# Optimization experiments

Measured on AMD Instinct MI355X. Metric: run time of the kernel, lower is better.

Reference implementation:

```python
import jax, jax.numpy as jnp
import numpy as np

N = 10000
E = 320000
IN, HID, OUT = 512, 128, 128
HEADS, GC = 4, 64
NEG_SLOPE = 0.2


def setup_inputs() -> dict:
    key = jax.random.key(0)
    ks = jax.random.split(key, 12)
    inp = {
        'x': jax.random.normal(ks[0], (N, IN), dtype=jnp.float32),
        'edge_index': jax.random.randint(ks[1], (2, E), 0, N, dtype=jnp.int64),
        # encoder params
        'W1': jax.random.normal(ks[2], (IN, HID), dtype=jnp.float32) / np.sqrt(IN),
        'b1': jnp.zeros((HID,), dtype=jnp.float32),
        'W2': jax.random.normal(ks[3], (HID, OUT), dtype=jnp.float32) / np.sqrt(HID),
        'b2': jnp.zeros((OUT,), dtype=jnp.float32),
        # GATConv params: lin weight [OUT, HEADS*GC], att vectors [HEADS, GC], bias [HEADS*GC]
        'Wg': jax.random.normal(ks[4], (OUT, HEADS * GC), dtype=jnp.float32) / np.sqrt(OUT),
        'att_src': jax.random.normal(ks[5], (HEADS, GC), dtype=jnp.float32) * 0.1,
        'att_dst': jax.random.normal(ks[6], (HEADS, GC), dtype=jnp.float32) * 0.1,
        'bias_g': jnp.zeros((HEADS * GC,), dtype=jnp.float32),
    }
    return inp


def _forward(x, W1, b1, W2, b2, Wg, att_src, att_dst, bias_g, edge_index):
    # encoder: Linear -> ReLU -> Linear
    h = jax.nn.relu(x @ W1 + b1) @ W2 + b2  # [N, OUT]
    # GATConv adds self-loops by default
    loops = jnp.arange(N, dtype=edge_index.dtype)
    src = jnp.concatenate([edge_index[0], loops])  # message sources j
    dst = jnp.concatenate([edge_index[1], loops])  # message targets i
    # per-head linear transform
    g = (h @ Wg).reshape(N, HEADS, GC)  # [N, H, C]
    a_src = jnp.sum(g * att_src, axis=-1)  # [N, H]
    a_dst = jnp.sum(g * att_dst, axis=-1)  # [N, H]
    e = a_src[src] + a_dst[dst]            # [E+N, H]
    e = jax.nn.leaky_relu(e, NEG_SLOPE)
    # segment softmax over incoming edges of each destination node
    m = jax.ops.segment_max(e, dst, num_segments=N)  # [N, H]
    ex = jnp.exp(e - m[dst])
    s = jax.ops.segment_sum(ex, dst, num_segments=N)  # [N, H]
    alpha = ex / s[dst]                    # [E+N, H]
    # weighted scatter-aggregate of source features
    out = jax.ops.segment_sum(g[src] * alpha[:, :, None], dst, num_segments=N)  # [N, H, C]
    return out.reshape(N, HEADS * GC) + bias_g


def reference(x, edge_index, W1, b1, W2, b2, Wg, att_src, att_dst, bias_g):
    return _forward(x, W1, b1, W2, b2, Wg, att_src, att_dst, bias_g, edge_index)
```

## Files before the change

kernel.cpp:

```cpp
#include <hip/hip_runtime.h>

#define N_NODES 10000
#define N_EDGES 320000
#define DIM_IN  512
#define DIM_HID 128
#define HC      256
#define NEG_SLOPE 0.2f
#define SLOT    96

typedef short short8 __attribute__((ext_vector_type(8)));
typedef float floatx4 __attribute__((ext_vector_type(4)));

__device__ __forceinline__ unsigned short f2bf(float x) {
  unsigned int u = __float_as_uint(x);
  u += 0x7FFFu + ((u >> 16) & 1u);
  return (unsigned short)(u >> 16);
}

union Sm1 {
  struct { unsigned short As[64][48]; unsigned short Bs[32][48]; } g;
  struct { float Ast[16][68]; float Bsf[16][64]; } p;
};

__global__ __launch_bounds__(256) void fused1_kernel(
    const float* __restrict__ x, const float* __restrict__ W1,
    const float* __restrict__ b1,
    const float* __restrict__ W2, const float* __restrict__ Wg,
    const float* __restrict__ b2,
    unsigned short* __restrict__ h1b, unsigned short* __restrict__ WfT,
    float* __restrict__ bfuse, int* __restrict__ cursor) {
  __shared__ Sm1 sm;
  const int t = threadIdx.x;
  const int b = blockIdx.x;

  if (b < 628) {
    constexpr int K = DIM_IN, N = DIM_HID, BK = 32;
    const int m0 = (b % 157) * 64, n0 = (b / 157) * 32;
    const int w = t >> 6, L = t & 63, lm = L & 15, q = L >> 4;
    floatx4 acc[2] = {};
    const int ar = t >> 3, ac = (t & 7) * 4;
    float4 va0, va1, vb, va0n, va1n, vbn;
    auto ld = [&](int kb, float4& a0, float4& a1, float4& bw) {
      a0 = (m0 + ar < N_NODES)
          ? *(const float4*)(x + (size_t)(m0 + ar) * K + kb + ac)
          : make_float4(0.f, 0.f, 0.f, 0.f);
      a1 = (m0 + ar + 32 < N_NODES)
          ? *(const float4*)(x + (size_t)(m0 + ar + 32) * K + kb + ac)
          : make_float4(0.f, 0.f, 0.f, 0.f);
      bw = *(const float4*)(W1 + (size_t)(kb + ar) * N + n0 + ac);
    };
    constexpr int NT = K / BK;
    ld(0, va0, va1, vb);
    for (int kt = 0; kt < NT; ++kt) {
      ushort4 s0 = {f2bf(va0.x), f2bf(va0.y), f2bf(va0.z), f2bf(va0.w)};
      ushort4 s1 = {f2bf(va1.x), f2bf(va1.y), f2bf(va1.z), f2bf(va1.w)};
      *(ushort4*)&sm.g.As[ar][ac]      = s0;
      *(ushort4*)&sm.g.As[ar + 32][ac] = s1;
      sm.g.Bs[ac + 0][ar] = f2bf(vb.x);
      sm.g.Bs[ac + 1][ar] = f2bf(vb.y);
      sm.g.Bs[ac + 2][ar] = f2bf(vb.z);
      sm.g.Bs[ac + 3][ar] = f2bf(vb.w);
      __syncthreads();
      if (kt + 1 < NT) ld((kt + 1) * BK, va0n, va1n, vbn);
      const short8 af = *(const short8*)&sm.g.As[w * 16 + lm][q * 8];
#pragma unroll
      for (int nt = 0; nt < 2; ++nt) {
        const short8 bf = *(const short8*)&sm.g.Bs[nt * 16 + lm][q * 8];
        acc[nt] = __builtin_amdgcn_mfma_f32_16x16x32_bf16(af, bf, acc[nt], 0, 0, 0);
      }
      __syncthreads();
      va0 = va0n; va1 = va1n; vb = vbn;
    }
    const int row0 = m0 + w * 16 + q * 4;
#pragma unroll
    for (int nt = 0; nt < 2; ++nt) {
      const int col = n0 + nt * 16 + lm;
      const float bv = b1[col];
#pragma unroll
      for (int r = 0; r < 4; ++r)
        if (row0 + r < N_NODES)
          h1b[(size_t)(row0 + r) * N + col] = f2bf(fmaxf(acc[nt][r] + bv, 0.f));
    }
    return;
  }

  const int bp = b - 628;
  {
    const int flat = bp * 256 + t;
    if (flat < (N_NODES + 3) / 4) ((int4*)cursor)[flat] = make_int4(0, 0, 0, 0);
  }
  const int bx = bp >> 2, by = bp & 3;
  const int tx = t & 15, ty = t >> 4;
  const int m0 = bx * 64, n0 = by * 64;
  const int ar = t >> 2, ac4 = (t & 3) * 4;
  const int br = t >> 4, bc4 = (t & 15) * 4;
  const int arow = m0 + ar;
  float acc[4][4] = {};
  float4 av, bv, avn, bvn;
  auto gload = [&](int k0, float4& a4, float4& b4) {
    if (arow < DIM_HID)       a4 = *(const float4*)(W2 + (size_t)arow * DIM_HID + k0 + ac4);
    else if (arow == DIM_HID) a4 = *(const float4*)(b2 + k0 + ac4);
    else                      a4 = make_float4(0.f, 0.f, 0.f, 0.f);
    b4 = *(const float4*)(Wg + (size_t)(k0 + br) * HC + n0 + bc4);
  };
  gload(0, av, bv);
  for (int k0 = 0; k0 < DIM_HID; k0 += 16) {
    sm.p.Ast[ac4 + 0][ar] = av.x; sm.p.Ast[ac4 + 1][ar] = av.y;
    sm.p.Ast[ac4 + 2][ar] = av.z; sm.p.Ast[ac4 + 3][ar] = av.w;
    *(float4*)&sm.p.Bsf[br][bc4] = bv;
    __syncthreads();
    if (k0 + 16 < DIM_HID) gload(k0 + 16, avn, bvn);
#pragma unroll
    for (int kk = 0; kk < 16; ++kk) {
      const float4 a = *(const float4*)&sm.p.Ast[kk][ty * 4];
      const float4 bq = *(const float4*)&sm.p.Bsf[kk][tx * 4];
      const float as[4] = {a.x, a.y, a.z, a.w};
      const float bs[4] = {bq.x, bq.y, bq.z, bq.w};
#pragma unroll
      for (int i = 0; i < 4; ++i)
#pragma unroll
        for (int j = 0; j < 4; ++j) acc[i][j] = fmaf(as[i], bs[j], acc[i][j]);
    }
    __syncthreads();
    av = avn; bv = bvn;
  }
#pragma unroll
  for (int i = 0; i < 4; ++i) {
    const int row = m0 + ty * 4 + i;
#pragma unroll
    for (int j = 0; j < 4; ++j) {
      const int col = n0 + tx * 4 + j;
      if (row < DIM_HID)       WfT[(size_t)col * DIM_HID + row] = f2bf(acc[i][j]);
      else if (row == DIM_HID) bfuse[col] = acc[i][j];
    }
  }
}

__global__ __launch_bounds__(256) void gemm2_kernel(
    const unsigned short* __restrict__ h1b, const unsigned short* __restrict__ WfT,
    const float* __restrict__ bfuse, unsigned short* __restrict__ g,
    const float* __restrict__ att_src, const float* __restrict__ att_dst,
    float* __restrict__ a_src, float* __restrict__ a_dst,
    const int* __restrict__ e_src, const int* __restrict__ e_dst,
    int* __restrict__ cursor, int* __restrict__ src_sorted) {
  constexpr int K = DIM_HID, N = HC, BK = 32;
  __shared__ unsigned short As[64][48];
  __shared__ unsigned short Bs[64][48];
  const int t = threadIdx.x;
  {
    const int nthr = gridDim.x * gridDim.y * 256;
    const int flat = (blockIdx.y * gridDim.x + blockIdx.x) * 256 + t;
    for (int id = flat; id < N_EDGES + N_NODES; id += nthr) {
      int s, d;
      if (id < N_EDGES) { s = e_src[id]; d = e_dst[id]; }
      else              { s = d = id - N_EDGES; }
      src_sorted[d * SLOT + atomicAdd(&cursor[d], 1)] = s;
    }
  }
  const int m0 = blockIdx.x * 64, n0 = blockIdx.y * 64;
  const int w = t >> 6, L = t & 63, lm = L & 15, q = L >> 4;
  floatx4 acc[4] = {};
  uint4 ab, abn, bb, bbn;
  auto ld = [&](int kb, uint4& va, uint4& vb) {
    va = *(const uint4*)(h1b + (size_t)(m0 + (t >> 2)) * K + kb + (t & 3) * 8);
    vb = *(const uint4*)(WfT + (size_t)(n0 + (t >> 2)) * K + kb + (t & 3) * 8);
  };
  constexpr int NT = K / BK;
  ld(0, ab, bb);
  for (int kt = 0; kt < NT; ++kt) {
    *(uint4*)&As[t >> 2][(t & 3) * 8] = ab;
    *(uint4*)&Bs[t >> 2][(t & 3) * 8] = bb;
    __syncthreads();
    if (kt + 1 < NT) ld((kt + 1) * BK, abn, bbn);
    const short8 af = *(const short8*)&As[w * 16 + lm][q * 8];
#pragma unroll
    for (int nt = 0; nt < 4; ++nt) {
      const short8 bf = *(const short8*)&Bs[nt * 16 + lm][q * 8];
      acc[nt] = __builtin_amdgcn_mfma_f32_16x16x32_bf16(af, bf, acc[nt], 0, 0, 0);
    }
    __syncthreads();
    ab = abn; bb = bbn;
  }
  const int row0 = m0 + w * 16 + q * 4;
  const int hh = n0 >> 6;
  float ps[4] = {}, pd[4] = {};
#pragma unroll
  for (int nt = 0; nt < 4; ++nt) {
    const int col = n0 + nt * 16 + lm;
    const float bv = bfuse[col];
    const float as_c = att_src[hh * 64 + nt * 16 + lm];
    const float ad_c = att_dst[hh * 64 + nt * 16 + lm];
#pragma unroll
    for (int r = 0; r < 4; ++r) {
      const float gv = acc[nt][r] + bv;
      if (row0 + r < N_NODES) g[(size_t)(row0 + r) * N + col] = f2bf(gv);
      ps[r] = fmaf(gv, as_c, ps[r]);
      pd[r] = fmaf(gv, ad_c, pd[r]);
    }
  }
#pragma unroll
  for (int r = 0; r < 4; ++r) {
#pragma unroll
    for (int off = 1; off < 16; off <<= 1) {
      ps[r] += __shfl_xor(ps[r], off);
      pd[r] += __shfl_xor(pd[r], off);
    }
    if (lm == 0 && row0 + r < N_NODES) {
      a_src[(row0 + r) * 4 + hh] = ps[r];
      a_dst[(row0 + r) * 4 + hh] = pd[r];
    }
  }
}

__global__ __launch_bounds__(256) void aggregate_kernel(
    const unsigned short* __restrict__ g, const float* __restrict__ a_src,
    const float* __restrict__ a_dst, const int* __restrict__ cursor,
    const int* __restrict__ src_sorted, const float* __restrict__ bias_g,
    float* __restrict__ out) {
  const int wv   = threadIdx.x >> 6;
  const int lane = threadIdx.x & 63;
  const int node = blockIdx.x * 4 + wv;
  if (node >= N_NODES) return;
  const int e2 = lane >> 5;
  const int c8 = lane & 31;
  const int h  = c8 >> 3;
  const int start = node * SLOT;
  const int end   = start + cursor[node];
  const float4 ad = *(const float4*)(a_dst + node * 4);

  float a[8] = {};
  float s_loc = 0.f;
  for (int base = start; base < end; base += 64) {
    const int rem = min(64, end - base);
    int   sidxL = 0;
    float w0 = 0.f, w1 = 0.f, w2 = 0.f, w3 = 0.f;
    if (lane < rem) {
      sidxL = src_sorted[base + lane];
      const float4 as4 = *(const float4*)(a_src + sidxL * 4);
      float e0 = as4.x + ad.x; e0 = (e0 > 0.f) ? e0 : NEG_SLOPE * e0;
      float e1 = as4.y + ad.y; e1 = (e1 > 0.f) ? e1 : NEG_SLOPE * e1;
      float ee = as4.z + ad.z; ee = (ee > 0.f) ? ee : NEG_SLOPE * ee;
      float e3 = as4.w + ad.w; e3 = (e3 > 0.f) ? e3 : NEG_SLOPE * e3;
      w0 = __expf(e0); w1 = __expf(e1); w2 = __expf(ee); w3 = __expf(e3);
    }
    const int half = (rem + 1) >> 1;
#pragma unroll 4
    for (int k = 0; k < half; ++k) {
      const int j  = 2 * k + e2;
      const int js = (j < rem) ? j : (rem - 1);
      const int sj = __shfl(sidxL, js);
      const float f0 = __shfl(w0, js), f1 = __shfl(w1, js);
      const float f2 = __shfl(w2, js), f3 = __shfl(w3, js);
      float w = (h & 2) ? ((h & 1) ? f3 : f2) : ((h & 1) ? f1 : f0);
      if (j >= rem) w = 0.f;
      const uint4 gv = *(const uint4*)(g + (size_t)sj * HC + c8 * 8);
      s_loc += w;
      a[0] = fmaf(w, __uint_as_float(gv.x << 16), a[0]);
      a[1] = fmaf(w, __uint_as_float(gv.x & 0xFFFF0000u), a[1]);
      a[2] = fmaf(w, __uint_as_float(gv.y << 16), a[2]);
      a[3] = fmaf(w, __uint_as_float(gv.y & 0xFFFF0000u), a[3]);
      a[4] = fmaf(w, __uint_as_float(gv.z << 16), a[4]);
      a[5] = fmaf(w, __uint_as_float(gv.z & 0xFFFF0000u), a[5]);
      a[6] = fmaf(w, __uint_as_float(gv.w << 16), a[6]);
      a[7] = fmaf(w, __uint_as_float(gv.w & 0xFFFF0000u), a[7]);
    }
  }
#pragma unroll
  for (int k = 0; k < 8; ++k) a[k] += __shfl_xor(a[k], 32);
  s_loc += __shfl_xor(s_loc, 32);
  if (e2 == 0) {
    const float inv = 1.f / s_loc;
    const float4 b0 = *(const float4*)(bias_g + c8 * 8);
    const float4 b1v = *(const float4*)(bias_g + c8 * 8 + 4);
    float4 o0, o1;
    o0.x = a[0] * inv + b0.x;  o0.y = a[1] * inv + b0.y;
    o0.z = a[2] * inv + b0.z;  o0.w = a[3] * inv + b0.w;
    o1.x = a[4] * inv + b1v.x; o1.y = a[5] * inv + b1v.y;
    o1.z = a[6] * inv + b1v.z; o1.w = a[7] * inv + b1v.w;
    float* op = out + (size_t)node * HC + c8 * 8;
    *(float4*)op = o0;
    *(float4*)(op + 4) = o1;
  }
}

extern "C" void kernel_launch(void* const* d_in, const int* in_sizes, int n_in,
                              void* d_out, int out_size, void* d_ws, size_t ws_size,
                              hipStream_t stream) {
  const float* x       = (const float*)d_in[0];
  const int*   ei      = (const int*)d_in[1];
  const float* W1      = (const float*)d_in[2];
  const float* b1      = (const float*)d_in[3];
  const float* W2      = (const float*)d_in[4];
  const float* b2      = (const float*)d_in[5];
  const float* Wg      = (const float*)d_in[6];
  const float* att_src = (const float*)d_in[7];
  const float* att_dst = (const float*)d_in[8];
  const float* bias_g  = (const float*)d_in[9];
  float* out = (float*)d_out;

  char* ws = (char*)d_ws;
  unsigned short* h1b = (unsigned short*)ws; ws += (size_t)(N_NODES + 64) * DIM_HID * 2;
  unsigned short* g   = (unsigned short*)ws; ws += (size_t)N_NODES * HC * 2;
  unsigned short* WfT = (unsigned short*)ws; ws += (size_t)HC * DIM_HID * 2;
  float* bfuse   = (float*)ws; ws += (size_t)HC * 4;
  float* a_src   = (float*)ws; ws += (size_t)N_NODES * 4 * 4;
  float* a_dst   = (float*)ws; ws += (size_t)N_NODES * 4 * 4;
  int* cursor    = (int*)ws;   ws += (size_t)N_NODES * 4;
  int* src_sorted= (int*)ws;   ws += (size_t)N_NODES * SLOT * 4;

  const dim3 blk(256);
  fused1_kernel<<<640, blk, 0, stream>>>(
      x, W1, b1, W2, Wg, b2, h1b, WfT, bfuse, cursor);
  gemm2_kernel<<<dim3(157, 4), blk, 0, stream>>>(
      h1b, WfT, bfuse, g, att_src, att_dst, a_src, a_dst,
      ei, ei + N_EDGES, cursor, src_sorted);
  aggregate_kernel<<<(N_NODES + 3) / 4, blk, 0, stream>>>(
      g, a_src, a_dst, cursor, src_sorted, bias_g, out);
}
```

Before: 152.7 us.

## Stage edge weights in LDS and gather four edges per wave step

The aggregation kernel now computes each edge's softmax numerators and source index once per wave, stores them in shared memory, and reads them back. This replaces the per-edge shuffle broadcasts. Each lane now covers 16 channels with two 16-byte loads, so one wave processes four edges per iteration instead of two, which adds gather parallelism. The cost is more registers for the wider accumulator, an extra cross-lane reduction step, and a block-wide barrier. The node bounds check is removed, which depends on N being a multiple of 4 and on degree never exceeding SLOT.

New measurement: 147.5 us. -3.4%, faster.

```diff
diff --git a/kernel.cpp b/kernel.cpp
--- a/kernel.cpp
+++ b/kernel.cpp
@@ -217,69 +217,87 @@
     const float* __restrict__ a_dst, const int* __restrict__ cursor,
     const int* __restrict__ src_sorted, const float* __restrict__ bias_g,
     float* __restrict__ out) {
+  __shared__ int   s_idx[4][SLOT];
+  __shared__ float s_w[4][SLOT * 4];
   const int wv   = threadIdx.x >> 6;
   const int lane = threadIdx.x & 63;
   const int node = blockIdx.x * 4 + wv;
-  if (node >= N_NODES) return;
-  const int e2 = lane >> 5;
-  const int c8 = lane & 31;
-  const int h  = c8 >> 3;
   const int start = node * SLOT;
-  const int end   = start + cursor[node];
+  const int deg   = cursor[node];
+  const int degp  = (deg + 3) & ~3;
   const float4 ad = *(const float4*)(a_dst + node * 4);
 
-  float a[8] = {};
-  float s_loc = 0.f;
-  for (int base = start; base < end; base += 64) {
-    const int rem = min(64, end - base);
-    int   sidxL = 0;
+  for (int j = lane; j < degp; j += 64) {
+    int   s  = 0;
     float w0 = 0.f, w1 = 0.f, w2 = 0.f, w3 = 0.f;
-    if (lane < rem) {
-      sidxL = src_sorted[base + lane];
-      const float4 as4 = *(const float4*)(a_src + sidxL * 4);
+    if (j < deg) {
+      s = src_sorted[start + j];
+      const float4 as4 = *(const float4*)(a_src + s * 4);
       float e0 = as4.x + ad.x; e0 = (e0 > 0.f) ? e0 : NEG_SLOPE * e0;
       float e1 = as4.y + ad.y; e1 = (e1 > 0.f) ? e1 : NEG_SLOPE * e1;
-      float ee = as4.z + ad.z; ee = (ee > 0.f) ? ee : NEG_SLOPE * ee;
+      float e2v = as4.z + ad.z; e2v = (e2v > 0.f) ? e2v : NEG_SLOPE * e2v;
       float e3 = as4.w + ad.w; e3 = (e3 > 0.f) ? e3 : NEG_SLOPE * e3;
-      w0 = __expf(e0); w1 = __expf(e1); w2 = __expf(ee); w3 = __expf(e3);
-    }
-    const int half = (rem + 1) >> 1;
-#pragma unroll 4
-    for (int k = 0; k < half; ++k) {
-      const int j  = 2 * k + e2;
-      const int js = (j < rem) ? j : (rem - 1);
-      const int sj = __shfl(sidxL, js);
-      const float f0 = __shfl(w0, js), f1 = __shfl(w1, js);
-      const float f2 = __shfl(w2, js), f3 = __shfl(w3, js);
-      float w = (h & 2) ? ((h & 1) ? f3 : f2) : ((h & 1) ? f1 : f0);
-      if (j >= rem) w = 0.f;
-      const uint4 gv = *(const uint4*)(g + (size_t)sj * HC + c8 * 8);
-      s_loc += w;
-      a[0] = fmaf(w, __uint_as_float(gv.x << 16), a[0]);
-      a[1] = fmaf(w, __uint_as_float(gv.x & 0xFFFF0000u), a[1]);
-      a[2] = fmaf(w, __uint_as_float(gv.y << 16), a[2]);
-      a[3] = fmaf(w, __uint_as_float(gv.y & 0xFFFF0000u), a[3]);
-      a[4] = fmaf(w, __uint_as_float(gv.z << 16), a[4]);
-      a[5] = fmaf(w, __uint_as_float(gv.z & 0xFFFF0000u), a[5]);
-      a[6] = fmaf(w, __uint_as_float(gv.w << 16), a[6]);
-      a[7] = fmaf(w, __uint_as_float(gv.w & 0xFFFF0000u), a[7]);
-    }
-  }
-#pragma unroll
-  for (int k = 0; k < 8; ++k) a[k] += __shfl_xor(a[k], 32);
+      w0 = __expf(e0); w1 = __expf(e1); w2 = __expf(e2v); w3 = __expf(e3);
+    }
+    s_idx[wv][j] = s;
+    float* wp = &s_w[wv][j * 4];
+    wp[0] = w0; wp[1] = w1; wp[2] = w2; wp[3] = w3;
+  }
+  __syncthreads();
+
+  const int e4 = lane >> 4;
+  const int c4 = lane & 15;
+  const int h  = c4 >> 2;
+  const unsigned short* gbase = g + (size_t)c4 * 16;
+  float a[16] = {};
+  float s_loc = 0.f;
+  const int iters = degp >> 2;
+#pragma unroll 2
+  for (int k = 0; k < iters; ++k) {
+    const int j  = 4 * k + e4;
+    const int sj = s_idx[wv][j];
+    const float w = s_w[wv][j * 4 + h];
+    const uint4 g0 = *(const uint4*)(gbase + (size_t)sj * HC);
+    const uint4 g1 = *(const uint4*)(gbase + (size_t)sj * HC + 8);
+    s_loc += w;
+    a[0]  = fmaf(w, __uint_as_float(g0.x << 16),         a[0]);
+    a[1]  = fmaf(w, __uint_as_float(g0.x & 0xFFFF0000u), a[1]);
+    a[2]  = fmaf(w, __uint_as_float(g0.y << 16),         a[2]);
+    a[3]  = fmaf(w, __uint_as_float(g0.y & 0xFFFF0000u), a[3]);
+    a[4]  = fmaf(w, __uint_as_float(g0.z << 16),         a[4]);
+    a[5]  = fmaf(w, __uint_as_float(g0.z & 0xFFFF0000u), a[5]);
+    a[6]  = fmaf(w, __uint_as_float(g0.w << 16),         a[6]);
+    a[7]  = fmaf(w, __uint_as_float(g0.w & 0xFFFF0000u), a[7]);
+    a[8]  = fmaf(w, __uint_as_float(g1.x << 16),         a[8]);
+    a[9]  = fmaf(w, __uint_as_float(g1.x & 0xFFFF0000u), a[9]);
+    a[10] = fmaf(w, __uint_as_float(g1.y << 16),         a[10]);
+    a[11] = fmaf(w, __uint_as_float(g1.y & 0xFFFF0000u), a[11]);
+    a[12] = fmaf(w, __uint_as_float(g1.z << 16),         a[12]);
+    a[13] = fmaf(w, __uint_as_float(g1.z & 0xFFFF0000u), a[13]);
+    a[14] = fmaf(w, __uint_as_float(g1.w << 16),         a[14]);
+    a[15] = fmaf(w, __uint_as_float(g1.w & 0xFFFF0000u), a[15]);
+  }
+#pragma unroll
+  for (int k = 0; k < 16; ++k) {
+    a[k] += __shfl_xor(a[k], 16);
+    a[k] += __shfl_xor(a[k], 32);
+  }
+  s_loc += __shfl_xor(s_loc, 16);
   s_loc += __shfl_xor(s_loc, 32);
-  if (e2 == 0) {
+  if (e4 == 0) {
     const float inv = 1.f / s_loc;
-    const float4 b0 = *(const float4*)(bias_g + c8 * 8);
-    const float4 b1v = *(const float4*)(bias_g + c8 * 8 + 4);
-    float4 o0, o1;
-    o0.x = a[0] * inv + b0.x;  o0.y = a[1] * inv + b0.y;
-    o0.z = a[2] * inv + b0.z;  o0.w = a[3] * inv + b0.w;
-    o1.x = a[4] * inv + b1v.x; o1.y = a[5] * inv + b1v.y;
-    o1.z = a[6] * inv + b1v.z; o1.w = a[7] * inv + b1v.w;
-    float* op = out + (size_t)node * HC + c8 * 8;
-    *(float4*)op = o0;
-    *(float4*)(op + 4) = o1;
+    float* op = out + (size_t)node * HC + c4 * 16;
+    const float* bp = bias_g + c4 * 16;
+#pragma unroll
+    for (int q = 0; q < 4; ++q) {
+      const float4 bq = *(const float4*)(bp + q * 4);
+      float4 o;
+      o.x = a[4 * q + 0] * inv + bq.x;
+      o.y = a[4 * q + 1] * inv + bq.y;
+      o.z = a[4 * q + 2] * inv + bq.z;
+      o.w = a[4 * q + 3] * inv + bq.w;
+      *(float4*)(op + q * 4) = o;
+    }
   }
 }
 
@@ -314,6 +332,6 @@
   gemm2_kernel<<<dim3(157, 4), blk, 0, stream>>>(
       h1b, WfT, bfuse, g, att_src, att_dst, a_src, a_dst,
       ei, ei + N_EDGES, cursor, src_sorted);
-  aggregate_kernel<<<(N_NODES + 3) / 4, blk, 0, stream>>>(
+  aggregate_kernel<<<N_NODES / 4, blk, 0, stream>>>(
       g, a_src, a_dst, cursor, src_sorted, bias_g, out);
 }
```
